# Performance work log

Hardware: AMD Instinct MI355X
Metric: run time of the kernel (lower is better)

The kernel has to match this reference:

```python
import jax, jax.numpy as jnp
import numpy as np

N_QUBITS = 8
N_LAYERS = 2
DIM = 2 ** N_QUBITS  # 256


def _ry(theta):
    h = theta * 0.5
    c, s = jnp.cos(h), jnp.sin(h)
    return jnp.stack([jnp.stack([c, -s]), jnp.stack([s, c])]).astype(jnp.complex64)


def _rz(theta):
    e = jnp.exp(-0.5j * theta.astype(jnp.complex64))
    z = jnp.zeros((), jnp.complex64)
    return jnp.stack([jnp.stack([e, z]), jnp.stack([z, jnp.conj(e)])])


def _apply_1q(state, U, w):
    # state: (2,)*n tensor, wire 0 = most significant (PennyLane convention)
    s = jnp.moveaxis(state, w, 0)
    s = jnp.tensordot(U, s, axes=((1,), (0,)))
    return jnp.moveaxis(s, 0, w)


def _cnot(state, c, t):
    s = jnp.moveaxis(state, (c, t), (0, 1))
    s = jnp.stack([s[0, 0], s[0, 1], s[1, 1], s[1, 0]]).reshape((2, 2) + s.shape[2:])
    return jnp.moveaxis(s, (0, 1), (c, t))


def _conv_pair(state, q1, q2, p):
    state = _apply_1q(state, _ry(p[0]), q1)
    state = _apply_1q(state, _ry(p[1]), q2)
    state = _cnot(state, q1, q2)
    state = _apply_1q(state, _ry(p[2]), q1)
    state = _apply_1q(state, _ry(p[3]), q2)
    state = _cnot(state, q2, q1)
    return state


def _circuit(angles, node_idx, adj, qp):
    n = N_QUBITS
    state = jnp.zeros((2,) * n, jnp.complex64).at[(0,) * n].set(1.0)
    a = jnp.clip(angles, -np.pi, np.pi)
    # angle encoding: RY on all wires, RZ on wires 0..n/2-1
    for i in range(n):
        state = _apply_1q(state, _ry(a[i]), i)
    for i in range(n // 2):
        state = _apply_1q(state, _rz(a[i + n // 2]), i)
    # graph-structure entanglement: conditional CNOT(c=node%n, t) if adj[c,t]>0
    c = (node_idx % n).astype(jnp.int32)
    adj_row = adj[c]
    flat = state.reshape(-1)
    idx = jnp.arange(DIM, dtype=jnp.int32)
    bit_c = (idx >> (n - 1 - c)) & 1  # dynamic control wire
    for t in range(n):
        perm = idx ^ (bit_c << (n - 1 - t))
        cond = (adj_row[t] > 0) & (t != c)
        flat = jnp.where(cond, flat[perm], flat)
    state = flat.reshape((2,) * n)
    # quantum conv layers
    ppc = 4 * (n - 1)
    off = 0
    for _ in range(N_LAYERS):
        p = qp[off:off + ppc]
        k = 0
        for i in range(0, n - 1, 2):
            state = _conv_pair(state, i, i + 1, p[k:k + 4]); k += 4
        for i in range(1, n - 1, 2):
            state = _conv_pair(state, i, i + 1, p[k:k + 4]); k += 4
        off += ppc
    # pooling rotations on even wires
    pool = qp[off:off + n]
    for q in range(0, n, 2):
        state = _apply_1q(state, _ry(pool[q]), q)
    # <Z_w> expectation values
    probs = jnp.abs(state) ** 2
    z = jnp.stack([probs.take(0, axis=w).sum() - probs.take(1, axis=w).sum()
                   for w in range(n)])
    return z


def setup_inputs() -> dict:
    key = jax.random.key(0)
    ks = jax.random.split(key, 12)
    B, S, N, F = 64, 12, 207, 2
    x = jax.random.normal(ks[0], (B, S, N, F), jnp.float32)
    adj = jax.random.randint(ks[1], (N, N), 0, 2).astype(jnp.float32)
    w_proj = jax.random.normal(ks[2], (N_QUBITS, S * F), jnp.float32) * 0.1
    b_proj = jax.random.normal(ks[3], (N_QUBITS,), jnp.float32) * 0.1
    q_params = jax.random.normal(ks[4], (4 * (N_QUBITS - 1) * N_LAYERS + N_QUBITS,), jnp.float32) * 0.1
    w1 = jax.random.normal(ks[5], (64, N_QUBITS), jnp.float32) * 0.1
    b1 = jax.random.normal(ks[6], (64,), jnp.float32) * 0.1
    w2 = jax.random.normal(ks[7], (32, 64), jnp.float32) * 0.1
    b2 = jax.random.normal(ks[8], (32,), jnp.float32) * 0.1
    w3 = jax.random.normal(ks[9], (1, 32), jnp.float32) * 0.1
    b3 = jax.random.normal(ks[10], (1,), jnp.float32) * 0.1
    return dict(x=x, adj=adj, w_proj=w_proj, b_proj=b_proj, q_params=q_params,
                w1=w1, b1=b1, w2=w2, b2=b2, w3=w3, b3=b3)


def reference(x, adj, w_proj, b_proj, q_params, w1, b1, w2, b2, w3, b3):
    B, S, N, F = x.shape
    feats = jnp.transpose(x, (0, 2, 1, 3)).reshape(B, N, S * F)
    angles = feats @ w_proj.T + b_proj                      # (B, N, 8)
    node_idx = jnp.tile(jnp.arange(N, dtype=jnp.int32), B)  # (B*N,)
    z = jax.vmap(_circuit, in_axes=(0, 0, None, None))(
        angles.reshape(B * N, N_QUBITS), node_idx, adj, q_params)
    # original detaches quantum features before the classical head
    z = jax.lax.stop_gradient(z).reshape(B, N, N_QUBITS).astype(jnp.float32)
    h = jax.nn.relu(z @ w1.T + b1)   # dropout is identity in eval mode
    h = jax.nn.relu(h @ w2.T + b2)
    out = h @ w3.T + b3              # (B, N, 1)
    return out.squeeze(-1)
```

## Files before the change

kernel.cpp:

```cpp
#include <hip/hip_runtime.h>
#include <math.h>

#define DEV static __device__ __forceinline__

constexpr int SS = 12;
constexpr int NN = 207;
constexpr int NCIRC = 64 * NN;
constexpr int NPAIR = NCIRC / 2;


typedef float v2f __attribute__((ext_vector_type(2)));

DEV v2f splat2(float x) { v2f r; r.x = x; r.y = x; return r; }
DEV v2f vfma(float m, v2f a, v2f acc) { return __builtin_elementwise_fma(splat2(m), a, acc); }
DEV v2f vmul(float m, v2f a) { return splat2(m) * a; }
template<int M> DEV float sxc(float v) { return __shfl_xor(v, M, 64); }
template<int M> DEV v2f sx2(v2f v) { v2f r; r.x = sxc<M>(v.x); r.y = sxc<M>(v.y); return r; }

struct Ct { v2f a0, a1, a2, a3; };

DEV void convm(Ct& s, const float* __restrict__ P) {
    v2f b0 = s.a0, b1 = s.a1, b2 = s.a2, b3 = s.a3;
    s.a0 = vfma(P[0],  b0, vfma(P[1],  b1, vfma(P[2],  b2, vmul(P[3],  b3))));
    s.a1 = vfma(P[4],  b0, vfma(P[5],  b1, vfma(P[6],  b2, vmul(P[7],  b3))));
    s.a2 = vfma(P[8],  b0, vfma(P[9],  b1, vfma(P[10], b2, vmul(P[11], b3))));
    s.a3 = vfma(P[12], b0, vfma(P[13], b1, vfma(P[14], b2, vmul(P[15], b3))));
}

template<int J> DEV void swkl1(Ct& s, int lane) {
    const bool lb = (lane >> J) & 1;
    v2f t0 = sx2<(1 << J)>(s.a2), t1 = sx2<(1 << J)>(s.a3);
    v2f t2 = sx2<(1 << J)>(s.a0), t3 = sx2<(1 << J)>(s.a1);
    s.a0 = lb ? t0 : s.a0; s.a1 = lb ? t1 : s.a1;
    s.a2 = lb ? s.a2 : t2; s.a3 = lb ? s.a3 : t3;
}

template<int J> DEV void swkl0(Ct& s, int lane) {
    const bool lb = (lane >> J) & 1;
    v2f t0 = sx2<(1 << J)>(s.a1), t1 = sx2<(1 << J)>(s.a0);
    v2f t2 = sx2<(1 << J)>(s.a3), t3 = sx2<(1 << J)>(s.a2);
    s.a0 = lb ? t0 : s.a0; s.a1 = lb ? s.a1 : t1;
    s.a2 = lb ? t2 : s.a2; s.a3 = lb ? s.a3 : t3;
}

template<int J> DEV void ryl(Ct& s, int lane, float c, float sv) {
    const float sg = ((lane >> J) & 1) ? sv : -sv;
    v2f p;
    p = sx2<(1 << J)>(s.a0); s.a0 = __builtin_elementwise_fma(splat2(c), s.a0, vmul(sg, p));
    p = sx2<(1 << J)>(s.a1); s.a1 = __builtin_elementwise_fma(splat2(c), s.a1, vmul(sg, p));
    p = sx2<(1 << J)>(s.a2); s.a2 = __builtin_elementwise_fma(splat2(c), s.a2, vmul(sg, p));
    p = sx2<(1 << J)>(s.a3); s.a3 = __builtin_elementwise_fma(splat2(c), s.a3, vmul(sg, p));
}

DEV Ct init_state(const float* __restrict__ xp, const float* __restrict__ w_proj,
                  const float* __restrict__ b_proj, int lane) {
    v2f av[8];
#pragma unroll
    for (int k = 0; k < 8; k++) av[k] = splat2(0.0f);
#pragma unroll
    for (int s = 0; s < SS; s++) {
        const v2f xv = *(const v2f*)(xp + (size_t)s * (NN * 2));
#pragma unroll
        for (int k = 0; k < 8; k++) {
            const v2f wv2 = *(const v2f*)(w_proj + k * 24 + 2 * s);
            av[k] = __builtin_elementwise_fma(xv, wv2, av[k]);
        }
    }
    const float PI_F = 3.14159265358979323846f;
    float ang[8];
#pragma unroll
    for (int k = 0; k < 8; k++)
        ang[k] = fminf(fmaxf(av[k].x + av[k].y + b_proj[k], -PI_F), PI_F);
    float cc[8], ssn[8];
#pragma unroll
    for (int i = 0; i < 8; i++) __sincosf(0.5f * ang[i], &ssn[i], &cc[i]);
    float A = 1.0f;
#pragma unroll
    for (int i = 0; i < 6; i++)
        A *= ((lane >> (5 - i)) & 1) ? ssn[i] : cc[i];
    float phi = 0.0f;
#pragma unroll
    for (int i = 0; i < 4; i++)
        phi += ((lane >> (5 - i)) & 1) ? 0.5f * ang[4 + i] : -0.5f * ang[4 + i];
    float cp, sp;
    __sincosf(phi, &sp, &cp);
    v2f ph; ph.x = cp; ph.y = sp;
    Ct s;
    s.a0 = vmul(A * cc[6] * cc[7], ph);
    s.a1 = vmul(A * cc[6] * ssn[7], ph);
    s.a2 = vmul(A * ssn[6] * cc[7], ph);
    s.a3 = vmul(A * ssn[6] * ssn[7], ph);
    return s;
}

DEV Ct adj_gather(const Ct& s, int Mlane, int Mlo) {
    v2f p0, p1, p2, p3;
    if (Mlo == 0)      { p0 = s.a0; p1 = s.a1; p2 = s.a2; p3 = s.a3; }
    else if (Mlo == 1) { p0 = s.a1; p1 = s.a0; p2 = s.a3; p3 = s.a2; }
    else if (Mlo == 2) { p0 = s.a2; p1 = s.a3; p2 = s.a0; p3 = s.a1; }
    else               { p0 = s.a3; p1 = s.a2; p2 = s.a1; p3 = s.a0; }
    p0.x = __shfl_xor(p0.x, Mlane, 64); p0.y = __shfl_xor(p0.y, Mlane, 64);
    p1.x = __shfl_xor(p1.x, Mlane, 64); p1.y = __shfl_xor(p1.y, Mlane, 64);
    p2.x = __shfl_xor(p2.x, Mlane, 64); p2.y = __shfl_xor(p2.y, Mlane, 64);
    p3.x = __shfl_xor(p3.x, Mlane, 64); p3.y = __shfl_xor(p3.y, Mlane, 64);
    Ct r; r.a0 = p0; r.a1 = p1; r.a2 = p2; r.a3 = p3;
    return r;
}

DEV void adj_select(Ct& s, const Ct& p, int pc, int lane) {
    if (pc >= 2) {
        const bool bb = (lane >> (pc - 2)) & 1;
        s.a0 = bb ? p.a0 : s.a0; s.a1 = bb ? p.a1 : s.a1;
        s.a2 = bb ? p.a2 : s.a2; s.a3 = bb ? p.a3 : s.a3;
    } else if (pc == 1) { s.a2 = p.a2; s.a3 = p.a3; }
    else                { s.a1 = p.a1; s.a3 = p.a3; }
}

DEV void build_z(const Ct& s, int lane, v2f& za, v2f& zb, v2f& zc, v2f& zd) {
    const float p0 = fmaf(s.a0.x, s.a0.x, s.a0.y * s.a0.y);
    const float p1 = fmaf(s.a1.x, s.a1.x, s.a1.y * s.a1.y);
    const float p2 = fmaf(s.a2.x, s.a2.x, s.a2.y * s.a2.y);
    const float p3 = fmaf(s.a3.x, s.a3.x, s.a3.y * s.a3.y);
    const float psum = (p0 + p1) + (p2 + p3);
    za.x = ((lane >> 1) & 1) ? -psum : psum;
    za.y = ((lane >> 2) & 1) ? -psum : psum;
    zb.x = ((lane >> 5) & 1) ? -psum : psum;
    zb.y = (lane & 1)        ? -psum : psum;
    zc.x = ((lane >> 3) & 1) ? -psum : psum;
    zc.y = (p0 - p1) + (p2 - p3);
    zd.x = (p0 + p1) - (p2 + p3);
    zd.y = ((lane >> 4) & 1) ? -psum : psum;
#define BFLY(MM) do { za += sx2<MM>(za); zb += sx2<MM>(zb);               \
                      zc += sx2<MM>(zc); zd += sx2<MM>(zd); } while (0)
    BFLY(1); BFLY(2); BFLY(4); BFLY(8); BFLY(16); BFLY(32);
#undef BFLY
}

__global__ void prep_kernel(const float* __restrict__ qp, float* __restrict__ ws) {
    const int n = threadIdx.x;
    if (n == 14) {
        float s, c;
        sincosf(0.5f * qp[56], &s, &c); ws[224] = c; ws[225] = s;
        sincosf(0.5f * qp[58], &s, &c); ws[226] = c; ws[227] = s;
        sincosf(0.5f * qp[60], &s, &c); ws[228] = c; ws[229] = s;
    }
    if (n >= 14) return;
    const int Jt[14] = {12, 8, 24, 4, 20, 0, 16, 32, 28, 44, 36, 48, 40, 52};
    const int Vt[14] = { 0, 0,  1, 0,  1, 0,  1,  0,  0,  1,  0,  1,  0,  1};
    const int J = Jt[n], v = Vt[n];
    float cg[4], sg[4];
    for (int i = 0; i < 4; i++) sincosf(0.5f * qp[J + i], &sg[i], &cg[i]);
    const int h1i = v ? 1 : 0, l1i = v ? 0 : 1;
    const int h2i = v ? 3 : 2, l2i = v ? 2 : 3;
    float A[16], B[16], M[16];
    {
        float H[2][2] = {{cg[h1i], -sg[h1i]}, {sg[h1i], cg[h1i]}};
        float L[2][2] = {{cg[l1i], -sg[l1i]}, {sg[l1i], cg[l1i]}};
        for (int a = 0; a < 2; a++) for (int b = 0; b < 2; b++)
            for (int p = 0; p < 2; p++) for (int q = 0; q < 2; q++)
                A[(2*a+b)*4 + (2*p+q)] = H[a][p] * L[b][q];
    }
    { const int ra = v ? 1 : 2;
      for (int j = 0; j < 4; j++) { float t = A[ra*4+j]; A[ra*4+j] = A[12+j]; A[12+j] = t; } }
    {
        float H[2][2] = {{cg[h2i], -sg[h2i]}, {sg[h2i], cg[h2i]}};
        float L[2][2] = {{cg[l2i], -sg[l2i]}, {sg[l2i], cg[l2i]}};
        for (int a = 0; a < 2; a++) for (int b = 0; b < 2; b++)
            for (int p = 0; p < 2; p++) for (int q = 0; q < 2; q++)
                B[(2*a+b)*4 + (2*p+q)] = H[a][p] * L[b][q];
    }
    for (int r = 0; r < 4; r++)
        for (int cl = 0; cl < 4; cl++) {
            float acc = 0.0f;
            for (int k = 0; k < 4; k++) acc += B[r*4+k] * A[k*4+cl];
            M[r*4+cl] = acc;
        }
    { const int rb = v ? 2 : 1;
      for (int j = 0; j < 4; j++) { float t = M[rb*4+j]; M[rb*4+j] = M[12+j]; M[12+j] = t; } }
    if (n == 13) {
        float ps, pc;
        sincosf(0.5f * qp[62], &ps, &pc);
        for (int j = 0; j < 4; j++) {
            float r0 = M[j],   r2 = M[8+j];
            M[j]   = pc * r0 - ps * r2;  M[8+j]  = ps * r0 + pc * r2;
            float r1 = M[4+j], r3 = M[12+j];
            M[4+j] = pc * r1 - ps * r3;  M[12+j] = ps * r1 + pc * r3;
        }
    }
    for (int i = 0; i < 16; i++) ws[16*n + i] = M[i];
}

__global__ __launch_bounds__(256) void qcnn_kernel(
    const float* __restrict__ x, const float* __restrict__ adj,
    const float* __restrict__ w_proj, const float* __restrict__ b_proj,
    const float* __restrict__ ws,
    const float* __restrict__ w1, const float* __restrict__ b1,
    const float* __restrict__ w2, const float* __restrict__ b2,
    const float* __restrict__ w3, const float* __restrict__ b3,
    float* __restrict__ out)
{
    const int lane = threadIdx.x & 63;
    const int wv   = threadIdx.x >> 6;
    const int gA   = blockIdx.x * 4 + wv;
    const int gB   = gA + NPAIR;
    const int bA   = gA / NN;
    const int node = gA - bA * NN;

    const float* xpA = x + ((size_t)bA * SS * NN + node) * 2;
    const float* xpB = xpA + (size_t)32 * SS * NN * 2;

    Ct sA = init_state(xpA, w_proj, b_proj, lane);
    Ct sB = init_state(xpB, w_proj, b_proj, lane);

    const int cq = node & 7;
    int M = 0;
#pragma unroll
    for (int t = 0; t < 8; t++) {
        float avv = adj[cq * NN + t];
        if (t != cq && avv > 0.0f) M |= 1 << (7 - t);
    }
    if (M) {
        const int Mlane = M >> 2, Mlo = M & 3, pc = 7 - cq;
        Ct pA = adj_gather(sA, Mlane, Mlo);
        Ct pB = adj_gather(sB, Mlane, Mlo);
        adj_select(sA, pA, pc, lane);
        adj_select(sB, pB, pc, lane);
    }

#define C2(OFF)  do { convm(sA, ws + (OFF)); convm(sB, ws + (OFF)); } while (0)
#define S12(J)   do { swkl1<J>(sA, lane); swkl1<J>(sB, lane); } while (0)
#define S02(J)   do { swkl0<J>(sA, lane); swkl0<J>(sB, lane); } while (0)
    C2(0);
    S12(1); S02(0);
    C2(16);
    S12(1);
    C2(32);
    S12(3); S02(2);
    C2(48);
    S12(1);
    C2(64);
    S12(5); S02(4);
    C2(80);
    S12(1);
    C2(96);
    S02(4);
    C2(112);
    S12(1); S02(4);
    C2(128);
    S12(1);
    C2(144);
    S12(5); S02(2);
    C2(160);
    S02(4);
    C2(176);
    S12(3); S02(0);
    C2(192);
    S02(4);
    C2(208);
#undef C2
#undef S12
#undef S02

    ryl<1>(sA, lane, ws[224], ws[225]); ryl<1>(sB, lane, ws[224], ws[225]);
    ryl<5>(sA, lane, ws[226], ws[227]); ryl<5>(sB, lane, ws[226], ws[227]);
    ryl<3>(sA, lane, ws[228], ws[229]); ryl<3>(sB, lane, ws[228], ws[229]);

    v2f zaA, zbA, zcA, zdA, zaB, zbB, zcB, zdB;
    build_z(sA, lane, zaA, zbA, zcA, zdA);
    build_z(sB, lane, zaB, zbB, zcB, zdB);

    const v2f* w1v = (const v2f*)(w1 + lane * 8);
    const v2f w10 = w1v[0], w11 = w1v[1], w12 = w1v[2], w13 = w1v[3];
    v2f hA = zaA * w10;
    hA = __builtin_elementwise_fma(zbA, w11, hA);
    hA = __builtin_elementwise_fma(zcA, w12, hA);
    hA = __builtin_elementwise_fma(zdA, w13, hA);
    v2f hB = zaB * w10;
    hB = __builtin_elementwise_fma(zbB, w11, hB);
    hB = __builtin_elementwise_fma(zcB, w12, hB);
    hB = __builtin_elementwise_fma(zdB, w13, hB);
    const float bb1 = b1[lane];
    const float h1A = fmaxf(bb1 + hA.x + hA.y, 0.0f);
    const float h1B = fmaxf(bb1 + hB.x + hB.y, 0.0f);

    __shared__ float h1s[8][64];
    h1s[2 * wv][lane]     = h1A;
    h1s[2 * wv + 1][lane] = h1B;

    const int m = lane & 31;
    const v2f* hsv = (const v2f*)(&h1s[2 * wv + (lane >> 5)][0]);
    const v2f* w2v = (const v2f*)(w2 + m * 64);
    v2f acc2 = splat2(0.0f);
#pragma unroll
    for (int j = 0; j < 32; j++)
        acc2 = __builtin_elementwise_fma(hsv[j], w2v[j], acc2);
    const float h2 = fmaxf(b2[m] + acc2.x + acc2.y, 0.0f);

    float o = h2 * w3[m];
    o += sxc<1>(o); o += sxc<2>(o); o += sxc<4>(o); o += sxc<8>(o); o += sxc<16>(o);

    if (m == 0) out[(lane >> 5) ? gB : gA] = o + b3[0];
}

extern "C" void kernel_launch(void* const* d_in, const int* in_sizes, int n_in,
                              void* d_out, int out_size, void* d_ws, size_t ws_size,
                              hipStream_t stream) {
    const float* x      = (const float*)d_in[0];
    const float* adj    = (const float*)d_in[1];
    const float* w_proj = (const float*)d_in[2];
    const float* b_proj = (const float*)d_in[3];
    const float* qp     = (const float*)d_in[4];
    const float* w1     = (const float*)d_in[5];
    const float* b1     = (const float*)d_in[6];
    const float* w2     = (const float*)d_in[7];
    const float* b2     = (const float*)d_in[8];
    const float* w3     = (const float*)d_in[9];
    const float* b3     = (const float*)d_in[10];
    float* out = (float*)d_out;
    float* ws  = (float*)d_ws;

    hipLaunchKernelGGL(prep_kernel, dim3(1), dim3(64), 0, stream, qp, ws);
    hipLaunchKernelGGL(qcnn_kernel, dim3(NPAIR / 4), dim3(256), 0, stream,
                       x, adj, w_proj, b_proj, ws, w1, b1, w2, b2, w3, b3, out);
}
```

Before: 117.6 us.

## Halve shuffle traffic in swaps and compute Z expectations via Walsh-Hadamard butterfly

The swap helpers now select the outgoing pair before shuffling, so each lane-swap uses two vector shuffles instead of four. The final RY gates are applied after swapping those wires into register slots, so they need no shuffles. The Z-expectation reduction replaces eight sign-masked butterfly reductions with one Walsh-Hadamard butterfly on the total probability plus one two-wide reduction, then reads the needed coefficients with readlane. The second dense layer loads four floats at a time. The aim is to cut cross-lane shuffle cost in the epilogue, at the price of a more intricate correctness mapping between wires and lanes.

Measured after the change: 104.6 us. -11.1%, faster.

```diff
diff --git a/kernel.cpp b/kernel.cpp
--- a/kernel.cpp
+++ b/kernel.cpp
@@ -10,12 +10,16 @@
 
 
 typedef float v2f __attribute__((ext_vector_type(2)));
+typedef float v4f __attribute__((ext_vector_type(4)));
 
 DEV v2f splat2(float x) { v2f r; r.x = x; r.y = x; return r; }
 DEV v2f vfma(float m, v2f a, v2f acc) { return __builtin_elementwise_fma(splat2(m), a, acc); }
 DEV v2f vmul(float m, v2f a) { return splat2(m) * a; }
 template<int M> DEV float sxc(float v) { return __shfl_xor(v, M, 64); }
 template<int M> DEV v2f sx2(v2f v) { v2f r; r.x = sxc<M>(v.x); r.y = sxc<M>(v.y); return r; }
+DEV float rdl(float v, int l) {
+    return __int_as_float(__builtin_amdgcn_readlane(__float_as_int(v), l));
+}
 
 struct Ct { v2f a0, a1, a2, a3; };
 
@@ -29,27 +33,47 @@
 
 template<int J> DEV void swkl1(Ct& s, int lane) {
     const bool lb = (lane >> J) & 1;
-    v2f t0 = sx2<(1 << J)>(s.a2), t1 = sx2<(1 << J)>(s.a3);
-    v2f t2 = sx2<(1 << J)>(s.a0), t3 = sx2<(1 << J)>(s.a1);
-    s.a0 = lb ? t0 : s.a0; s.a1 = lb ? t1 : s.a1;
-    s.a2 = lb ? s.a2 : t2; s.a3 = lb ? s.a3 : t3;
+    v2f u0 = lb ? s.a0 : s.a2;
+    v2f u1 = lb ? s.a1 : s.a3;
+    v2f v0 = sx2<(1 << J)>(u0);
+    v2f v1 = sx2<(1 << J)>(u1);
+    s.a0 = lb ? v0 : s.a0;
+    s.a1 = lb ? v1 : s.a1;
+    s.a2 = lb ? s.a2 : v0;
+    s.a3 = lb ? s.a3 : v1;
 }
 
 template<int J> DEV void swkl0(Ct& s, int lane) {
     const bool lb = (lane >> J) & 1;
-    v2f t0 = sx2<(1 << J)>(s.a1), t1 = sx2<(1 << J)>(s.a0);
-    v2f t2 = sx2<(1 << J)>(s.a3), t3 = sx2<(1 << J)>(s.a2);
-    s.a0 = lb ? t0 : s.a0; s.a1 = lb ? s.a1 : t1;
-    s.a2 = lb ? t2 : s.a2; s.a3 = lb ? s.a3 : t3;
-}
-
-template<int J> DEV void ryl(Ct& s, int lane, float c, float sv) {
-    const float sg = ((lane >> J) & 1) ? sv : -sv;
-    v2f p;
-    p = sx2<(1 << J)>(s.a0); s.a0 = __builtin_elementwise_fma(splat2(c), s.a0, vmul(sg, p));
-    p = sx2<(1 << J)>(s.a1); s.a1 = __builtin_elementwise_fma(splat2(c), s.a1, vmul(sg, p));
-    p = sx2<(1 << J)>(s.a2); s.a2 = __builtin_elementwise_fma(splat2(c), s.a2, vmul(sg, p));
-    p = sx2<(1 << J)>(s.a3); s.a3 = __builtin_elementwise_fma(splat2(c), s.a3, vmul(sg, p));
+    v2f u0 = lb ? s.a0 : s.a1;
+    v2f u1 = lb ? s.a2 : s.a3;
+    v2f v0 = sx2<(1 << J)>(u0);
+    v2f v1 = sx2<(1 << J)>(u1);
+    s.a0 = lb ? v0 : s.a0;
+    s.a1 = lb ? s.a1 : v0;
+    s.a2 = lb ? v1 : s.a2;
+    s.a3 = lb ? s.a3 : v1;
+}
+
+DEV void ry_k0(Ct& s, float c, float sv) {
+    v2f b0 = s.a0, b2 = s.a2;
+    s.a0 = vfma(c, b0, vmul(-sv, s.a1));
+    s.a1 = vfma(sv, b0, vmul(c, s.a1));
+    s.a2 = vfma(c, b2, vmul(-sv, s.a3));
+    s.a3 = vfma(sv, b2, vmul(c, s.a3));
+}
+
+DEV void ry_k1(Ct& s, float c, float sv) {
+    v2f b0 = s.a0, b1 = s.a1;
+    s.a0 = vfma(c, b0, vmul(-sv, s.a2));
+    s.a2 = vfma(sv, b0, vmul(c, s.a2));
+    s.a1 = vfma(c, b1, vmul(-sv, s.a3));
+    s.a3 = vfma(sv, b1, vmul(c, s.a3));
+}
+
+template<int MK> DEV float whts(float p, int lane) {
+    float t = sxc<MK>(p);
+    return (lane & MK) ? (t - p) : (p + t);
 }
 
 DEV Ct init_state(const float* __restrict__ xp, const float* __restrict__ w_proj,
@@ -116,24 +140,19 @@
     else                { s.a1 = p.a1; s.a3 = p.a3; }
 }
 
-DEV void build_z(const Ct& s, int lane, v2f& za, v2f& zb, v2f& zc, v2f& zd) {
+DEV void build_z(const Ct& s, int lane, float& W, v2f& dk) {
     const float p0 = fmaf(s.a0.x, s.a0.x, s.a0.y * s.a0.y);
     const float p1 = fmaf(s.a1.x, s.a1.x, s.a1.y * s.a1.y);
     const float p2 = fmaf(s.a2.x, s.a2.x, s.a2.y * s.a2.y);
     const float p3 = fmaf(s.a3.x, s.a3.x, s.a3.y * s.a3.y);
-    const float psum = (p0 + p1) + (p2 + p3);
-    za.x = ((lane >> 1) & 1) ? -psum : psum;
-    za.y = ((lane >> 2) & 1) ? -psum : psum;
-    zb.x = ((lane >> 5) & 1) ? -psum : psum;
-    zb.y = (lane & 1)        ? -psum : psum;
-    zc.x = ((lane >> 3) & 1) ? -psum : psum;
-    zc.y = (p0 - p1) + (p2 - p3);
-    zd.x = (p0 + p1) - (p2 + p3);
-    zd.y = ((lane >> 4) & 1) ? -psum : psum;
-#define BFLY(MM) do { za += sx2<MM>(za); zb += sx2<MM>(zb);               \
-                      zc += sx2<MM>(zc); zd += sx2<MM>(zd); } while (0)
-    BFLY(1); BFLY(2); BFLY(4); BFLY(8); BFLY(16); BFLY(32);
-#undef BFLY
+    dk.x = (p0 - p1) + (p2 - p3);
+    dk.y = (p0 + p1) - (p2 + p3);
+    float w = (p0 + p1) + (p2 + p3);
+    w = whts<1>(w, lane);  w = whts<2>(w, lane);  w = whts<4>(w, lane);
+    w = whts<8>(w, lane);  w = whts<16>(w, lane); w = whts<32>(w, lane);
+    W = w;
+    dk += sx2<1>(dk);  dk += sx2<2>(dk);  dk += sx2<4>(dk);
+    dk += sx2<8>(dk);  dk += sx2<16>(dk); dk += sx2<32>(dk);
 }
 
 __global__ void prep_kernel(const float* __restrict__ qp, float* __restrict__ ws) {
@@ -261,40 +280,48 @@
 #undef S12
 #undef S02
 
-    ryl<1>(sA, lane, ws[224], ws[225]); ryl<1>(sB, lane, ws[224], ws[225]);
-    ryl<5>(sA, lane, ws[226], ws[227]); ryl<5>(sB, lane, ws[226], ws[227]);
-    ryl<3>(sA, lane, ws[228], ws[229]); ryl<3>(sB, lane, ws[228], ws[229]);
-
-    v2f zaA, zbA, zcA, zdA, zaB, zbB, zcB, zdB;
-    build_z(sA, lane, zaA, zbA, zcA, zdA);
-    build_z(sB, lane, zaB, zbB, zcB, zdB);
-
-    const v2f* w1v = (const v2f*)(w1 + lane * 8);
-    const v2f w10 = w1v[0], w11 = w1v[1], w12 = w1v[2], w13 = w1v[3];
-    v2f hA = zaA * w10;
-    hA = __builtin_elementwise_fma(zbA, w11, hA);
-    hA = __builtin_elementwise_fma(zcA, w12, hA);
-    hA = __builtin_elementwise_fma(zdA, w13, hA);
-    v2f hB = zaB * w10;
-    hB = __builtin_elementwise_fma(zbB, w11, hB);
-    hB = __builtin_elementwise_fma(zcB, w12, hB);
-    hB = __builtin_elementwise_fma(zdB, w13, hB);
-    const float bb1 = b1[lane];
-    const float h1A = fmaxf(bb1 + hA.x + hA.y, 0.0f);
-    const float h1B = fmaxf(bb1 + hB.x + hB.y, 0.0f);
+    swkl0<1>(sA, lane); swkl0<1>(sB, lane);
+    ry_k0(sA, ws[224], ws[225]); ry_k0(sB, ws[224], ws[225]);
+    swkl1<5>(sA, lane); swkl1<5>(sB, lane);
+    ry_k1(sA, ws[226], ws[227]); ry_k1(sB, ws[226], ws[227]);
+    swkl0<3>(sA, lane); swkl0<3>(sB, lane);
+    ry_k0(sA, ws[228], ws[229]); ry_k0(sB, ws[228], ws[229]);
+
+    float WA, WB; v2f dkA, dkB;
+    build_z(sA, lane, WA, dkA);
+    build_z(sB, lane, WB, dkB);
+    const float zA0 = rdl(WA, 8),  zA1 = rdl(WA, 4),  zA3 = rdl(WA, 1);
+    const float zA5 = rdl(WA, 2),  zA6 = rdl(WA, 32), zA7 = rdl(WA, 16);
+    const float zB0 = rdl(WB, 8),  zB1 = rdl(WB, 4),  zB3 = rdl(WB, 1);
+    const float zB5 = rdl(WB, 2),  zB6 = rdl(WB, 32), zB7 = rdl(WB, 16);
+
+    const v4f* w1q = (const v4f*)(w1 + lane * 8);
+    const v4f wLo = w1q[0], wHi = w1q[1];
+    float h1A = b1[lane];
+    h1A = fmaf(zA0, wLo.x, h1A); h1A = fmaf(zA1, wLo.y, h1A);
+    h1A = fmaf(dkA.y, wLo.z, h1A); h1A = fmaf(zA3, wLo.w, h1A);
+    h1A = fmaf(dkA.x, wHi.x, h1A); h1A = fmaf(zA5, wHi.y, h1A);
+    h1A = fmaf(zA6, wHi.z, h1A); h1A = fmaf(zA7, wHi.w, h1A);
+    float h1B = b1[lane];
+    h1B = fmaf(zB0, wLo.x, h1B); h1B = fmaf(zB1, wLo.y, h1B);
+    h1B = fmaf(dkB.y, wLo.z, h1B); h1B = fmaf(zB3, wLo.w, h1B);
+    h1B = fmaf(dkB.x, wHi.x, h1B); h1B = fmaf(zB5, wHi.y, h1B);
+    h1B = fmaf(zB6, wHi.z, h1B); h1B = fmaf(zB7, wHi.w, h1B);
+    h1A = fmaxf(h1A, 0.0f);
+    h1B = fmaxf(h1B, 0.0f);
 
     __shared__ float h1s[8][64];
     h1s[2 * wv][lane]     = h1A;
     h1s[2 * wv + 1][lane] = h1B;
 
     const int m = lane & 31;
-    const v2f* hsv = (const v2f*)(&h1s[2 * wv + (lane >> 5)][0]);
-    const v2f* w2v = (const v2f*)(w2 + m * 64);
-    v2f acc2 = splat2(0.0f);
-#pragma unroll
-    for (int j = 0; j < 32; j++)
-        acc2 = __builtin_elementwise_fma(hsv[j], w2v[j], acc2);
-    const float h2 = fmaxf(b2[m] + acc2.x + acc2.y, 0.0f);
+    const v4f* hsv = (const v4f*)(&h1s[2 * wv + (lane >> 5)][0]);
+    const v4f* w2v = (const v4f*)(w2 + m * 64);
+    v4f acc4 = {0.0f, 0.0f, 0.0f, 0.0f};
+#pragma unroll
+    for (int j = 0; j < 16; j++)
+        acc4 = __builtin_elementwise_fma(hsv[j], w2v[j], acc4);
+    const float h2 = fmaxf(b2[m] + (acc4.x + acc4.y) + (acc4.z + acc4.w), 0.0f);
 
     float o = h2 * w3[m];
     o += sxc<1>(o); o += sxc<2>(o); o += sxc<4>(o); o += sxc<8>(o); o += sxc<16>(o);
```

## Map each circuit to a half-wave with 8 amplitudes per lane

Applied to the files above, without the earlier changes.

Changes how the 256-amplitude state is laid out. Each 32-lane half-wave now holds one circuit with 8 amplitudes per lane, replacing the old scheme where each lane held 4 amplitudes for two circuits across the full wave. More of the two-qubit gates become register-local 4x4 multiplies with fewer cross-lane swaps. The expectation reductions now use a Walsh-Hadamard butterfly plus ds_bpermute, and the classical head is reworked with v4f loads. The trade-off is more registers per lane and a reordered gate schedule that must match the new prep matrix permutations.

Measured after the change: 118.0 us. About the same (+0.3%).

```diff
diff --git a/kernel.cpp b/kernel.cpp
--- a/kernel.cpp
+++ b/kernel.cpp
@@ -10,130 +10,60 @@
 
 
 typedef float v2f __attribute__((ext_vector_type(2)));
+typedef float v4f __attribute__((ext_vector_type(4)));
 
 DEV v2f splat2(float x) { v2f r; r.x = x; r.y = x; return r; }
 DEV v2f vfma(float m, v2f a, v2f acc) { return __builtin_elementwise_fma(splat2(m), a, acc); }
 DEV v2f vmul(float m, v2f a) { return splat2(m) * a; }
 template<int M> DEV float sxc(float v) { return __shfl_xor(v, M, 64); }
 template<int M> DEV v2f sx2(v2f v) { v2f r; r.x = sxc<M>(v.x); r.y = sxc<M>(v.y); return r; }
-
-struct Ct { v2f a0, a1, a2, a3; };
-
-DEV void convm(Ct& s, const float* __restrict__ P) {
-    v2f b0 = s.a0, b1 = s.a1, b2 = s.a2, b3 = s.a3;
-    s.a0 = vfma(P[0],  b0, vfma(P[1],  b1, vfma(P[2],  b2, vmul(P[3],  b3))));
-    s.a1 = vfma(P[4],  b0, vfma(P[5],  b1, vfma(P[6],  b2, vmul(P[7],  b3))));
-    s.a2 = vfma(P[8],  b0, vfma(P[9],  b1, vfma(P[10], b2, vmul(P[11], b3))));
-    s.a3 = vfma(P[12], b0, vfma(P[13], b1, vfma(P[14], b2, vmul(P[15], b3))));
-}
-
-template<int J> DEV void swkl1(Ct& s, int lane) {
-    const bool lb = (lane >> J) & 1;
-    v2f t0 = sx2<(1 << J)>(s.a2), t1 = sx2<(1 << J)>(s.a3);
-    v2f t2 = sx2<(1 << J)>(s.a0), t3 = sx2<(1 << J)>(s.a1);
-    s.a0 = lb ? t0 : s.a0; s.a1 = lb ? t1 : s.a1;
-    s.a2 = lb ? s.a2 : t2; s.a3 = lb ? s.a3 : t3;
-}
-
-template<int J> DEV void swkl0(Ct& s, int lane) {
-    const bool lb = (lane >> J) & 1;
-    v2f t0 = sx2<(1 << J)>(s.a1), t1 = sx2<(1 << J)>(s.a0);
-    v2f t2 = sx2<(1 << J)>(s.a3), t3 = sx2<(1 << J)>(s.a2);
-    s.a0 = lb ? t0 : s.a0; s.a1 = lb ? s.a1 : t1;
-    s.a2 = lb ? t2 : s.a2; s.a3 = lb ? s.a3 : t3;
-}
-
-template<int J> DEV void ryl(Ct& s, int lane, float c, float sv) {
-    const float sg = ((lane >> J) & 1) ? sv : -sv;
-    v2f p;
-    p = sx2<(1 << J)>(s.a0); s.a0 = __builtin_elementwise_fma(splat2(c), s.a0, vmul(sg, p));
-    p = sx2<(1 << J)>(s.a1); s.a1 = __builtin_elementwise_fma(splat2(c), s.a1, vmul(sg, p));
-    p = sx2<(1 << J)>(s.a2); s.a2 = __builtin_elementwise_fma(splat2(c), s.a2, vmul(sg, p));
-    p = sx2<(1 << J)>(s.a3); s.a3 = __builtin_elementwise_fma(splat2(c), s.a3, vmul(sg, p));
-}
-
-DEV Ct init_state(const float* __restrict__ xp, const float* __restrict__ w_proj,
-                  const float* __restrict__ b_proj, int lane) {
-    v2f av[8];
-#pragma unroll
-    for (int k = 0; k < 8; k++) av[k] = splat2(0.0f);
-#pragma unroll
-    for (int s = 0; s < SS; s++) {
-        const v2f xv = *(const v2f*)(xp + (size_t)s * (NN * 2));
-#pragma unroll
-        for (int k = 0; k < 8; k++) {
-            const v2f wv2 = *(const v2f*)(w_proj + k * 24 + 2 * s);
-            av[k] = __builtin_elementwise_fma(xv, wv2, av[k]);
-        }
-    }
-    const float PI_F = 3.14159265358979323846f;
-    float ang[8];
-#pragma unroll
-    for (int k = 0; k < 8; k++)
-        ang[k] = fminf(fmaxf(av[k].x + av[k].y + b_proj[k], -PI_F), PI_F);
-    float cc[8], ssn[8];
-#pragma unroll
-    for (int i = 0; i < 8; i++) __sincosf(0.5f * ang[i], &ssn[i], &cc[i]);
-    float A = 1.0f;
-#pragma unroll
-    for (int i = 0; i < 6; i++)
-        A *= ((lane >> (5 - i)) & 1) ? ssn[i] : cc[i];
-    float phi = 0.0f;
-#pragma unroll
-    for (int i = 0; i < 4; i++)
-        phi += ((lane >> (5 - i)) & 1) ? 0.5f * ang[4 + i] : -0.5f * ang[4 + i];
-    float cp, sp;
-    __sincosf(phi, &sp, &cp);
-    v2f ph; ph.x = cp; ph.y = sp;
-    Ct s;
-    s.a0 = vmul(A * cc[6] * cc[7], ph);
-    s.a1 = vmul(A * cc[6] * ssn[7], ph);
-    s.a2 = vmul(A * ssn[6] * cc[7], ph);
-    s.a3 = vmul(A * ssn[6] * ssn[7], ph);
-    return s;
-}
-
-DEV Ct adj_gather(const Ct& s, int Mlane, int Mlo) {
-    v2f p0, p1, p2, p3;
-    if (Mlo == 0)      { p0 = s.a0; p1 = s.a1; p2 = s.a2; p3 = s.a3; }
-    else if (Mlo == 1) { p0 = s.a1; p1 = s.a0; p2 = s.a3; p3 = s.a2; }
-    else if (Mlo == 2) { p0 = s.a2; p1 = s.a3; p2 = s.a0; p3 = s.a1; }
-    else               { p0 = s.a3; p1 = s.a2; p2 = s.a1; p3 = s.a0; }
-    p0.x = __shfl_xor(p0.x, Mlane, 64); p0.y = __shfl_xor(p0.y, Mlane, 64);
-    p1.x = __shfl_xor(p1.x, Mlane, 64); p1.y = __shfl_xor(p1.y, Mlane, 64);
-    p2.x = __shfl_xor(p2.x, Mlane, 64); p2.y = __shfl_xor(p2.y, Mlane, 64);
-    p3.x = __shfl_xor(p3.x, Mlane, 64); p3.y = __shfl_xor(p3.y, Mlane, 64);
-    Ct r; r.a0 = p0; r.a1 = p1; r.a2 = p2; r.a3 = p3;
-    return r;
-}
-
-DEV void adj_select(Ct& s, const Ct& p, int pc, int lane) {
-    if (pc >= 2) {
-        const bool bb = (lane >> (pc - 2)) & 1;
-        s.a0 = bb ? p.a0 : s.a0; s.a1 = bb ? p.a1 : s.a1;
-        s.a2 = bb ? p.a2 : s.a2; s.a3 = bb ? p.a3 : s.a3;
-    } else if (pc == 1) { s.a2 = p.a2; s.a3 = p.a3; }
-    else                { s.a1 = p.a1; s.a3 = p.a3; }
-}
-
-DEV void build_z(const Ct& s, int lane, v2f& za, v2f& zb, v2f& zc, v2f& zd) {
-    const float p0 = fmaf(s.a0.x, s.a0.x, s.a0.y * s.a0.y);
-    const float p1 = fmaf(s.a1.x, s.a1.x, s.a1.y * s.a1.y);
-    const float p2 = fmaf(s.a2.x, s.a2.x, s.a2.y * s.a2.y);
-    const float p3 = fmaf(s.a3.x, s.a3.x, s.a3.y * s.a3.y);
-    const float psum = (p0 + p1) + (p2 + p3);
-    za.x = ((lane >> 1) & 1) ? -psum : psum;
-    za.y = ((lane >> 2) & 1) ? -psum : psum;
-    zb.x = ((lane >> 5) & 1) ? -psum : psum;
-    zb.y = (lane & 1)        ? -psum : psum;
-    zc.x = ((lane >> 3) & 1) ? -psum : psum;
-    zc.y = (p0 - p1) + (p2 - p3);
-    zd.x = (p0 + p1) - (p2 + p3);
-    zd.y = ((lane >> 4) & 1) ? -psum : psum;
-#define BFLY(MM) do { za += sx2<MM>(za); zb += sx2<MM>(zb);               \
-                      zc += sx2<MM>(zc); zd += sx2<MM>(zd); } while (0)
-    BFLY(1); BFLY(2); BFLY(4); BFLY(8); BFLY(16); BFLY(32);
-#undef BFLY
+DEV float bperm(int addr, float v) {
+    return __int_as_float(__builtin_amdgcn_ds_bpermute(addr, __float_as_int(v)));
+}
+
+template<int BH, int BL>
+DEV void convm(v2f a[8], const float* __restrict__ P) {
+    constexpr int mh = 1 << BH, ml = 1 << BL;
+#pragma unroll
+    for (int j = 0; j < 8; j++) {
+        if (j & (mh | ml)) continue;
+        v2f b00 = a[j], b01 = a[j + ml], b10 = a[j + mh], b11 = a[j + mh + ml];
+        a[j]         = vfma(P[0],  b00, vfma(P[1],  b01, vfma(P[2],  b10, vmul(P[3],  b11))));
+        a[j + ml]    = vfma(P[4],  b00, vfma(P[5],  b01, vfma(P[6],  b10, vmul(P[7],  b11))));
+        a[j + mh]    = vfma(P[8],  b00, vfma(P[9],  b01, vfma(P[10], b10, vmul(P[11], b11))));
+        a[j + mh+ml] = vfma(P[12], b00, vfma(P[13], b01, vfma(P[14], b10, vmul(P[15], b11))));
+    }
+}
+
+template<int KB, int LB>
+DEV void swkl(v2f a[8], int lane) {
+    constexpr int m = 1 << KB, ML = 1 << LB;
+    const bool lb = (lane >> LB) & 1;
+#pragma unroll
+    for (int j = 0; j < 8; j++) {
+        if (j & m) continue;
+        v2f u = lb ? a[j] : a[j | m];
+        v2f v = sx2<ML>(u);
+        a[j]     = lb ? v : a[j];
+        a[j | m] = lb ? a[j | m] : v;
+    }
+}
+
+template<int KB>
+DEV void ry_k(v2f a[8], float c, float s) {
+    constexpr int m = 1 << KB;
+#pragma unroll
+    for (int j = 0; j < 8; j++) {
+        if (j & m) continue;
+        v2f lo = a[j], hi = a[j | m];
+        a[j]     = vfma(c, lo, vmul(-s, hi));
+        a[j | m] = vfma(s, lo, vmul(c, hi));
+    }
+}
+
+template<int MK> DEV float whts(float p, int lane) {
+    float t = sxc<MK>(p);
+    return (lane & MK) ? (t - p) : (p + t);
 }
 
 __global__ void prep_kernel(const float* __restrict__ qp, float* __restrict__ ws) {
@@ -145,47 +75,42 @@
         sincosf(0.5f * qp[60], &s, &c); ws[228] = c; ws[229] = s;
     }
     if (n >= 14) return;
-    const int Jt[14] = {12, 8, 24, 4, 20, 0, 16, 32, 28, 44, 36, 48, 40, 52};
-    const int Vt[14] = { 0, 0,  1, 0,  1, 0,  1,  0,  0,  1,  0,  1,  0,  1};
-    const int J = Jt[n], v = Vt[n];
+    const int Jt[14] = {12, 8, 24, 4, 20, 0, 16, 28, 32, 44, 36, 48, 40, 52};
+    const int J = Jt[n];
     float cg[4], sg[4];
     for (int i = 0; i < 4; i++) sincosf(0.5f * qp[J + i], &sg[i], &cg[i]);
-    const int h1i = v ? 1 : 0, l1i = v ? 0 : 1;
-    const int h2i = v ? 3 : 2, l2i = v ? 2 : 3;
     float A[16], B[16], M[16];
     {
-        float H[2][2] = {{cg[h1i], -sg[h1i]}, {sg[h1i], cg[h1i]}};
-        float L[2][2] = {{cg[l1i], -sg[l1i]}, {sg[l1i], cg[l1i]}};
-        for (int a = 0; a < 2; a++) for (int b = 0; b < 2; b++)
+        float H[2][2] = {{cg[0], -sg[0]}, {sg[0], cg[0]}};
+        float L[2][2] = {{cg[1], -sg[1]}, {sg[1], cg[1]}};
+        for (int a_ = 0; a_ < 2; a_++) for (int b_ = 0; b_ < 2; b_++)
             for (int p = 0; p < 2; p++) for (int q = 0; q < 2; q++)
-                A[(2*a+b)*4 + (2*p+q)] = H[a][p] * L[b][q];
-    }
-    { const int ra = v ? 1 : 2;
-      for (int j = 0; j < 4; j++) { float t = A[ra*4+j]; A[ra*4+j] = A[12+j]; A[12+j] = t; } }
+                A[(2*a_+b_)*4 + (2*p+q)] = H[a_][p] * L[b_][q];
+    }
+    for (int j = 0; j < 4; j++) { float t = A[8+j]; A[8+j] = A[12+j]; A[12+j] = t; }
     {
-        float H[2][2] = {{cg[h2i], -sg[h2i]}, {sg[h2i], cg[h2i]}};
-        float L[2][2] = {{cg[l2i], -sg[l2i]}, {sg[l2i], cg[l2i]}};
-        for (int a = 0; a < 2; a++) for (int b = 0; b < 2; b++)
+        float H[2][2] = {{cg[2], -sg[2]}, {sg[2], cg[2]}};
+        float L[2][2] = {{cg[3], -sg[3]}, {sg[3], cg[3]}};
+        for (int a_ = 0; a_ < 2; a_++) for (int b_ = 0; b_ < 2; b_++)
             for (int p = 0; p < 2; p++) for (int q = 0; q < 2; q++)
-                B[(2*a+b)*4 + (2*p+q)] = H[a][p] * L[b][q];
+                B[(2*a_+b_)*4 + (2*p+q)] = H[a_][p] * L[b_][q];
     }
     for (int r = 0; r < 4; r++)
-        for (int cl = 0; cl < 4; cl++) {
+        for (int c = 0; c < 4; c++) {
             float acc = 0.0f;
-            for (int k = 0; k < 4; k++) acc += B[r*4+k] * A[k*4+cl];
-            M[r*4+cl] = acc;
+            for (int k = 0; k < 4; k++) acc += B[r*4+k] * A[k*4+c];
+            M[r*4+c] = acc;
         }
-    { const int rb = v ? 2 : 1;
-      for (int j = 0; j < 4; j++) { float t = M[rb*4+j]; M[rb*4+j] = M[12+j]; M[12+j] = t; } }
+    for (int j = 0; j < 4; j++) { float t = M[4+j]; M[4+j] = M[12+j]; M[12+j] = t; }
     if (n == 13) {
         float ps, pc;
         sincosf(0.5f * qp[62], &ps, &pc);
-        for (int j = 0; j < 4; j++) {
-            float r0 = M[j],   r2 = M[8+j];
-            M[j]   = pc * r0 - ps * r2;  M[8+j]  = ps * r0 + pc * r2;
-            float r1 = M[4+j], r3 = M[12+j];
-            M[4+j] = pc * r1 - ps * r3;  M[12+j] = ps * r1 + pc * r3;
-        }
+        for (int g = 0; g < 4; g += 2)
+            for (int j = 0; j < 4; j++) {
+                float r0 = M[g*4+j], r1 = M[(g+1)*4+j];
+                M[g*4+j]     = pc * r0 - ps * r1;
+                M[(g+1)*4+j] = ps * r0 + pc * r1;
+            }
     }
     for (int i = 0; i < 16; i++) ws[16*n + i] = M[i];
 }
@@ -200,17 +125,56 @@
     float* __restrict__ out)
 {
     const int lane = threadIdx.x & 63;
+    const int half = lane >> 5;
+    const int hl   = lane & 31;
     const int wv   = threadIdx.x >> 6;
     const int gA   = blockIdx.x * 4 + wv;
-    const int gB   = gA + NPAIR;
     const int bA   = gA / NN;
     const int node = gA - bA * NN;
-
-    const float* xpA = x + ((size_t)bA * SS * NN + node) * 2;
-    const float* xpB = xpA + (size_t)32 * SS * NN * 2;
-
-    Ct sA = init_state(xpA, w_proj, b_proj, lane);
-    Ct sB = init_state(xpB, w_proj, b_proj, lane);
+    const int bb   = bA + (half << 5);
+
+    const float* xp = x + ((size_t)bb * SS * NN + node) * 2;
+    v2f av[8];
+#pragma unroll
+    for (int k = 0; k < 8; k++) av[k] = splat2(0.0f);
+#pragma unroll
+    for (int s = 0; s < SS; s++) {
+        const v2f xv = *(const v2f*)(xp + (size_t)s * (NN * 2));
+#pragma unroll
+        for (int k = 0; k < 8; k++) {
+            const v2f wv2 = *(const v2f*)(w_proj + k * 24 + 2 * s);
+            av[k] = __builtin_elementwise_fma(xv, wv2, av[k]);
+        }
+    }
+    const float PI_F = 3.14159265358979323846f;
+    float ang[8];
+#pragma unroll
+    for (int k = 0; k < 8; k++)
+        ang[k] = fminf(fmaxf(av[k].x + av[k].y + b_proj[k], -PI_F), PI_F);
+
+    float cc[8], ssn[8];
+#pragma unroll
+    for (int i = 0; i < 8; i++) __sincosf(0.5f * ang[i], &ssn[i], &cc[i]);
+    float A = 1.0f;
+#pragma unroll
+    for (int i = 0; i < 5; i++)
+        A *= ((lane >> (4 - i)) & 1) ? ssn[i] : cc[i];
+    float phi = 0.0f;
+#pragma unroll
+    for (int i = 0; i < 4; i++)
+        phi += ((lane >> (4 - i)) & 1) ? 0.5f * ang[4 + i] : -0.5f * ang[4 + i];
+    float cp, sp;
+    __sincosf(phi, &sp, &cp);
+    v2f ph; ph.x = cp; ph.y = sp;
+
+    v2f a[8];
+#pragma unroll
+    for (int k = 0; k < 8; k++) {
+        float coef = A * ((k & 4) ? ssn[5] : cc[5])
+                       * ((k & 2) ? ssn[6] : cc[6])
+                       * ((k & 1) ? ssn[7] : cc[7]);
+        a[k] = vmul(coef, ph);
+    }
 
     const int cq = node & 7;
     int M = 0;
@@ -220,86 +184,119 @@
         if (t != cq && avv > 0.0f) M |= 1 << (7 - t);
     }
     if (M) {
-        const int Mlane = M >> 2, Mlo = M & 3, pc = 7 - cq;
-        Ct pA = adj_gather(sA, Mlane, Mlo);
-        Ct pB = adj_gather(sB, Mlane, Mlo);
-        adj_select(sA, pA, pc, lane);
-        adj_select(sB, pB, pc, lane);
-    }
-
-#define C2(OFF)  do { convm(sA, ws + (OFF)); convm(sB, ws + (OFF)); } while (0)
-#define S12(J)   do { swkl1<J>(sA, lane); swkl1<J>(sB, lane); } while (0)
-#define S02(J)   do { swkl0<J>(sA, lane); swkl0<J>(sB, lane); } while (0)
-    C2(0);
-    S12(1); S02(0);
-    C2(16);
-    S12(1);
-    C2(32);
-    S12(3); S02(2);
-    C2(48);
-    S12(1);
-    C2(64);
-    S12(5); S02(4);
-    C2(80);
-    S12(1);
-    C2(96);
-    S02(4);
-    C2(112);
-    S12(1); S02(4);
-    C2(128);
-    S12(1);
-    C2(144);
-    S12(5); S02(2);
-    C2(160);
-    S02(4);
-    C2(176);
-    S12(3); S02(0);
-    C2(192);
-    S02(4);
-    C2(208);
-#undef C2
-#undef S12
-#undef S02
-
-    ryl<1>(sA, lane, ws[224], ws[225]); ryl<1>(sB, lane, ws[224], ws[225]);
-    ryl<5>(sA, lane, ws[226], ws[227]); ryl<5>(sB, lane, ws[226], ws[227]);
-    ryl<3>(sA, lane, ws[228], ws[229]); ryl<3>(sB, lane, ws[228], ws[229]);
-
-    v2f zaA, zbA, zcA, zdA, zaB, zbB, zcB, zdB;
-    build_z(sA, lane, zaA, zbA, zcA, zdA);
-    build_z(sB, lane, zaB, zbB, zcB, zdB);
-
-    const v2f* w1v = (const v2f*)(w1 + lane * 8);
-    const v2f w10 = w1v[0], w11 = w1v[1], w12 = w1v[2], w13 = w1v[3];
-    v2f hA = zaA * w10;
-    hA = __builtin_elementwise_fma(zbA, w11, hA);
-    hA = __builtin_elementwise_fma(zcA, w12, hA);
-    hA = __builtin_elementwise_fma(zdA, w13, hA);
-    v2f hB = zaB * w10;
-    hB = __builtin_elementwise_fma(zbB, w11, hB);
-    hB = __builtin_elementwise_fma(zcB, w12, hB);
-    hB = __builtin_elementwise_fma(zdB, w13, hB);
-    const float bb1 = b1[lane];
-    const float h1A = fmaxf(bb1 + hA.x + hA.y, 0.0f);
-    const float h1B = fmaxf(bb1 + hB.x + hB.y, 0.0f);
-
-    __shared__ float h1s[8][64];
-    h1s[2 * wv][lane]     = h1A;
-    h1s[2 * wv + 1][lane] = h1B;
-
-    const int m = lane & 31;
-    const v2f* hsv = (const v2f*)(&h1s[2 * wv + (lane >> 5)][0]);
-    const v2f* w2v = (const v2f*)(w2 + m * 64);
-    v2f acc2 = splat2(0.0f);
-#pragma unroll
-    for (int j = 0; j < 32; j++)
-        acc2 = __builtin_elementwise_fma(hsv[j], w2v[j], acc2);
-    const float h2 = fmaxf(b2[m] + acc2.x + acc2.y, 0.0f);
-
-    float o = h2 * w3[m];
+        const int Mlo = M & 7;
+        const int Mhi = (M >> 3) & 31;
+        v2f p[8];
+        switch (Mlo) {
+        case 0: p[0]=a[0];p[1]=a[1];p[2]=a[2];p[3]=a[3];p[4]=a[4];p[5]=a[5];p[6]=a[6];p[7]=a[7]; break;
+        case 1: p[0]=a[1];p[1]=a[0];p[2]=a[3];p[3]=a[2];p[4]=a[5];p[5]=a[4];p[6]=a[7];p[7]=a[6]; break;
+        case 2: p[0]=a[2];p[1]=a[3];p[2]=a[0];p[3]=a[1];p[4]=a[6];p[5]=a[7];p[6]=a[4];p[7]=a[5]; break;
+        case 3: p[0]=a[3];p[1]=a[2];p[2]=a[1];p[3]=a[0];p[4]=a[7];p[5]=a[6];p[6]=a[5];p[7]=a[4]; break;
+        case 4: p[0]=a[4];p[1]=a[5];p[2]=a[6];p[3]=a[7];p[4]=a[0];p[5]=a[1];p[6]=a[2];p[7]=a[3]; break;
+        case 5: p[0]=a[5];p[1]=a[4];p[2]=a[7];p[3]=a[6];p[4]=a[1];p[5]=a[0];p[6]=a[3];p[7]=a[2]; break;
+        case 6: p[0]=a[6];p[1]=a[7];p[2]=a[4];p[3]=a[5];p[4]=a[2];p[5]=a[3];p[6]=a[0];p[7]=a[1]; break;
+        default:p[0]=a[7];p[1]=a[6];p[2]=a[5];p[3]=a[4];p[4]=a[3];p[5]=a[2];p[6]=a[1];p[7]=a[0]; break;
+        }
+        const int addr = (lane ^ Mhi) << 2;
+#pragma unroll
+        for (int k = 0; k < 8; k++) {
+            p[k].x = bperm(addr, p[k].x);
+            p[k].y = bperm(addr, p[k].y);
+        }
+        const int pc = 7 - cq;
+        if (pc >= 3) {
+            const bool bsel = (lane >> (pc - 3)) & 1;
+#pragma unroll
+            for (int k = 0; k < 8; k++) a[k] = bsel ? p[k] : a[k];
+        } else if (pc == 2) { a[4]=p[4]; a[5]=p[5]; a[6]=p[6]; a[7]=p[7]; }
+        else if (pc == 1)   { a[2]=p[2]; a[3]=p[3]; a[6]=p[6]; a[7]=p[7]; }
+        else                { a[1]=p[1]; a[3]=p[3]; a[5]=p[5]; a[7]=p[7]; }
+    }
+
+    convm<1,0>(a, ws + 0);
+    swkl<0,0>(a, lane);
+    convm<0,2>(a, ws + 16);
+    convm<2,1>(a, ws + 32);
+    swkl<2,2>(a, lane);
+    swkl<1,1>(a, lane);
+    convm<2,1>(a, ws + 48);
+    convm<1,0>(a, ws + 64);
+    swkl<0,3>(a, lane);
+    swkl<1,4>(a, lane);
+    convm<1,0>(a, ws + 80);
+    convm<0,2>(a, ws + 96);
+    convm<1,0>(a, ws + 112);
+    swkl<1,4>(a, lane);
+    convm<2,1>(a, ws + 128);
+    convm<0,2>(a, ws + 144);
+    swkl<0,3>(a, lane);
+    swkl<2,2>(a, lane);
+    convm<0,2>(a, ws + 160);
+    convm<1,0>(a, ws + 176);
+    swkl<1,1>(a, lane);
+    swkl<0,0>(a, lane);
+    convm<1,0>(a, ws + 192);
+    convm<2,1>(a, ws + 208);
+
+    swkl<0,4>(a, lane);
+    ry_k<0>(a, ws[224], ws[225]);
+    swkl<1,2>(a, lane);
+    ry_k<1>(a, ws[226], ws[227]);
+    swkl<2,0>(a, lane);
+    ry_k<2>(a, ws[228], ws[229]);
+
+    float p0 = fmaf(a[0].x, a[0].x, a[0].y * a[0].y);
+    float p1 = fmaf(a[1].x, a[1].x, a[1].y * a[1].y);
+    float p2 = fmaf(a[2].x, a[2].x, a[2].y * a[2].y);
+    float p3 = fmaf(a[3].x, a[3].x, a[3].y * a[3].y);
+    float p4 = fmaf(a[4].x, a[4].x, a[4].y * a[4].y);
+    float p5 = fmaf(a[5].x, a[5].x, a[5].y * a[5].y);
+    float p6 = fmaf(a[6].x, a[6].x, a[6].y * a[6].y);
+    float p7 = fmaf(a[7].x, a[7].x, a[7].y * a[7].y);
+    const float s0 = p0 + p1, s1 = p2 + p3, s2 = p4 + p5, s3 = p6 + p7;
+    v2f z02;
+    z02.x = ((p0 - p1) + (p2 - p3)) + ((p4 - p5) + (p6 - p7));
+    z02.y = (s0 - s1) + (s2 - s3);
+    float z4p  = (s0 + s1) - (s2 + s3);
+    float w    = (s0 + s1) + (s2 + s3);
+    z02 += sx2<1>(z02);  z02 += sx2<2>(z02);  z02 += sx2<4>(z02);
+    z02 += sx2<8>(z02);  z02 += sx2<16>(z02);
+    z4p += sxc<1>(z4p);  z4p += sxc<2>(z4p);  z4p += sxc<4>(z4p);
+    z4p += sxc<8>(z4p);  z4p += sxc<16>(z4p);
+    w = whts<1>(w, lane); w = whts<2>(w, lane); w = whts<4>(w, lane);
+    w = whts<8>(w, lane); w = whts<16>(w, lane);
+    const int gb = (lane & 32) << 2;
+    const float z5 = bperm(gb | (1 << 2),  w);
+    const float z3 = bperm(gb | (2 << 2),  w);
+    const float z6 = bperm(gb | (4 << 2),  w);
+    const float z1 = bperm(gb | (8 << 2),  w);
+    const float z7 = bperm(gb | (16 << 2), w);
+    v4f zlo; zlo.x = z02.x; zlo.y = z1; zlo.z = z02.y; zlo.w = z3;
+    v4f zhi; zhi.x = z4p;   zhi.y = z5; zhi.z = z6;    zhi.w = z7;
+
+    const v4f* r0 = (const v4f*)(w1 + hl * 8);
+    const v4f* r1 = (const v4f*)(w1 + (hl + 32) * 8);
+    v4f ha = zlo * r0[0]; ha = __builtin_elementwise_fma(zhi, r0[1], ha);
+    v4f hb = zlo * r1[0]; hb = __builtin_elementwise_fma(zhi, r1[1], hb);
+    const float h1a = fmaxf(b1[hl]      + (ha.x + ha.y) + (ha.z + ha.w), 0.0f);
+    const float h1b = fmaxf(b1[hl + 32] + (hb.x + hb.y) + (hb.z + hb.w), 0.0f);
+
+    __shared__ float h1s[4][2][64];
+    h1s[wv][half][hl]      = h1a;
+    h1s[wv][half][hl + 32] = h1b;
+
+    const v4f* hv  = (const v4f*)(&h1s[wv][half][0]);
+    const v4f* w2r = (const v4f*)(w2 + hl * 64);
+    v4f acc = {0.0f, 0.0f, 0.0f, 0.0f};
+#pragma unroll
+    for (int j = 0; j < 16; j++)
+        acc = __builtin_elementwise_fma(hv[j], w2r[j], acc);
+    const float h2 = fmaxf(b2[hl] + (acc.x + acc.y) + (acc.z + acc.w), 0.0f);
+
+    float o = h2 * w3[hl];
     o += sxc<1>(o); o += sxc<2>(o); o += sxc<4>(o); o += sxc<8>(o); o += sxc<16>(o);
 
-    if (m == 0) out[(lane >> 5) ? gB : gA] = o + b3[0];
+    if (hl == 0) out[gA + half * NPAIR] = o + b3[0];
 }
 
 extern "C" void kernel_launch(void* const* d_in, const int* in_sizes, int n_in,
```
